# Optimization experiments

Measured on AMD Instinct MI355X. Metric: run time of the kernel, lower is better.

Reference implementation:

```python
import jax, jax.numpy as jnp
import numpy as np

N_TAXA = 32   # N taxa
K = 256       # particles
T = 16        # live subtrees at this step (t = N - r)
R = 16        # merges already done
S = 1024      # alignment sites
A = 4         # DNA alphabet
D = 64        # embedding dim
C = 16        # site-position feature dim
PRIOR_LEN = 0.1


def _expm4(M):
    """Matrix exponential of [..., A, A] via scaling-and-squaring + Taylor."""
    n_sq = 6
    Ms = M / (2.0 ** n_sq)
    I = jnp.eye(M.shape[-1], dtype=M.dtype)
    P = I + Ms
    Tm = Ms
    for i in range(2, 7):
        Tm = jnp.matmul(Tm, Ms) / i
        P = P + Tm
    for _ in range(n_sq):
        P = jnp.matmul(P, P)
    return P


def _stat_probs(emb_ExD, site_SxC, W_stat, W_site):
    # q_matrix_decoder.stat_probs_VxSxA: per-node, per-site stationary probs
    logits = emb_ExD @ W_stat                     # [E, A]
    logits = logits[:, None, :] + site_SxC @ W_site  # [E, S, A]
    return jax.nn.softmax(logits, axis=-1)


def setup_inputs() -> dict:
    key = jax.random.key(0)
    ks = jax.random.split(key, 10)
    ldf = np.zeros(2 * N_TAXA, np.float32)
    for n in range(2, 2 * N_TAXA):
        ldf[n] = ldf[n - 2] + np.log(n)
    return {
        "log_weight_K": jax.random.normal(ks[0], (K,), jnp.float32),
        "branch1_lengths_Kxr": jax.random.uniform(ks[1], (K, R), jnp.float32) * 0.2 + 1e-3,
        "branch2_lengths_Kxr": jax.random.uniform(ks[2], (K, R), jnp.float32) * 0.2 + 1e-3,
        "leaf_counts_Kxt": jnp.ones((K, T), jnp.int32),
        "embeddings_KxtxD": jax.random.normal(ks[3], (K, T, D), jnp.float32),
        "log_felsensteins_KxtxSxA": jax.nn.log_softmax(
            jax.random.normal(ks[4], (K, T, S, A), jnp.float32), axis=-1),
        "log_pi_K": jax.random.normal(ks[5], (K,), jnp.float32),
        "site_positions_SxC": jax.random.uniform(ks[6], (S, C), jnp.float32),
        "W_stat": jax.random.normal(ks[7], (D, A), jnp.float32) * 0.1,
        "W_site": jax.random.normal(ks[8], (C, A), jnp.float32) * 0.1,
        "log_double_factorials_2N": jnp.asarray(ldf),
    }


def reference(log_weight_K, branch1_lengths_Kxr, branch2_lengths_Kxr,
              leaf_counts_Kxt, embeddings_KxtxD, log_felsensteins_KxtxSxA,
              log_pi_K, site_positions_SxC, W_stat, W_site,
              log_double_factorials_2N):
    K_, T_, S_, A_ = log_felsensteins_KxtxSxA.shape
    key = jax.random.key(42)
    kres, ki, koff, ku1, ku2 = jax.random.split(key, 5)

    # ---- SMC categorical resampling over particles ----
    idxK = jax.random.categorical(kres, log_weight_K, shape=(K_,))
    b1r = branch1_lengths_Kxr[idxK]
    b2r = branch2_lengths_Kxr[idxK]
    lc = leaf_counts_Kxt[idxK]
    emb = embeddings_KxtxD[idxK]
    logf = log_felsensteins_KxtxSxA[idxK]
    prev_log_pi = log_pi_K[idxK]

    # ---- proposal (J=1): uniform pair + exponential branch lengths ----
    i = jax.random.randint(ki, (K_,), 0, T_)
    off = jax.random.randint(koff, (K_,), 1, T_)
    j = (i + off) % T_
    idx1 = jnp.minimum(i, j)
    idx2 = jnp.maximum(i, j)
    branch1 = -PRIOR_LEN * jnp.log(jax.random.uniform(ku1, (K_,), minval=1e-6, maxval=1.0))
    branch2 = -PRIOR_LEN * jnp.log(jax.random.uniform(ku2, (K_,), minval=1e-6, maxval=1.0))
    ar = jnp.arange(K_)
    new_emb = 0.5 * (emb[ar, idx1] + emb[ar, idx2])  # [K, D]
    log_v_plus = jnp.log(T_ * (T_ - 1) / 2.0)        # log #pairs

    # ---- merge: put merged value at idx1, move last slot into idx2, drop last ----
    def merge(arr, new_val):
        arr = arr.at[ar, idx1].set(new_val)
        arr = arr.at[ar, idx2].set(arr[ar, T_ - 1])
        return arr[:, :T_ - 1]

    lc_new = merge(lc, lc[ar, idx1] + lc[ar, idx2])   # [K, t-1]
    emb_new = merge(emb, new_emb)                     # [K, t-1, D]

    # ---- Felsenstein pruning step for the merged node ----
    stat = _stat_probs(new_emb, site_positions_SxC, W_stat, W_site)  # [K,S,A]
    Q = jnp.broadcast_to(stat[:, :, None, :], (K_, S_, A_, A_)) - jnp.eye(A_, dtype=stat.dtype)
    P1 = _expm4(Q * branch1[:, None, None, None])  # [K,S,A,A]
    P2 = _expm4(Q * branch2[:, None, None, None])
    f1 = jnp.exp(logf[ar, idx1])  # [K,S,A]
    f2 = jnp.exp(logf[ar, idx2])
    new_logf = (jnp.log(jnp.einsum('ksab,ksb->ksa', P1, f1) + 1e-30)
                + jnp.log(jnp.einsum('ksab,ksb->ksa', P2, f2) + 1e-30))
    logf_new = merge(logf, new_logf)  # [K, t-1, S, A]

    # ---- log pi over the forest: per-subtree likelihood + priors ----
    t_new = T_ - 1
    stat_all = _stat_probs(emb_new.reshape(K_ * t_new, -1), site_positions_SxC,
                           W_stat, W_site).reshape(K_, t_new, S_, A_)
    log_stat = jnp.log(stat_all)
    L = jnp.sum(jax.scipy.special.logsumexp(logf_new + log_stat, axis=-1), axis=-1)  # [K,t-1]
    topo_idx = jnp.clip(2 * lc_new - 3, 0, 2 * N_TAXA - 1)
    topo = -log_double_factorials_2N[topo_idx] * (lc_new >= 2).astype(L.dtype)
    b1_all = jnp.concatenate([b1r, branch1[:, None]], axis=1)  # [K, r+1]
    b2_all = jnp.concatenate([b2r, branch2[:, None]], axis=1)
    prior = (jnp.sum(-b1_all / PRIOR_LEN, axis=1) + jnp.sum(-b2_all / PRIOR_LEN, axis=1)
             - 2.0 * (b1_all.shape[1]) * jnp.log(jnp.asarray(PRIOR_LEN, L.dtype)))
    log_pi_new = jnp.sum(L + topo, axis=1) + prior

    # ---- importance weight ----
    log_v_minus = jnp.log(jnp.maximum(jnp.sum((lc_new > 1).astype(L.dtype), axis=1), 1.0))
    log_weight_new = log_pi_new - prev_log_pi + log_v_minus - log_v_plus
    return log_weight_new
```

## Files before the change

kernel.cpp:

```cpp
#include <hip/hip_runtime.h>
#include <stdint.h>


#define TF_ROT(x0,x1,r) { x0 += x1; x1 = ((x1<<(r))|(x1>>(32-(r)))); x1 ^= x0; }

__host__ __device__ inline void tf2x32(uint32_t k0, uint32_t k1,
                                       uint32_t x0, uint32_t x1,
                                       uint32_t& o0, uint32_t& o1) {
  uint32_t ks2 = k0 ^ k1 ^ 0x1BD11BDAu;
  x0 += k0; x1 += k1;
  TF_ROT(x0,x1,13) TF_ROT(x0,x1,15) TF_ROT(x0,x1,26) TF_ROT(x0,x1,6)
  x0 += k1; x1 += ks2 + 1u;
  TF_ROT(x0,x1,17) TF_ROT(x0,x1,29) TF_ROT(x0,x1,16) TF_ROT(x0,x1,24)
  x0 += ks2; x1 += k0 + 2u;
  TF_ROT(x0,x1,13) TF_ROT(x0,x1,15) TF_ROT(x0,x1,26) TF_ROT(x0,x1,6)
  x0 += k0; x1 += k1 + 3u;
  TF_ROT(x0,x1,17) TF_ROT(x0,x1,29) TF_ROT(x0,x1,16) TF_ROT(x0,x1,24)
  x0 += k1; x1 += ks2 + 4u;
  TF_ROT(x0,x1,13) TF_ROT(x0,x1,15) TF_ROT(x0,x1,26) TF_ROT(x0,x1,6)
  x0 += ks2; x1 += k0 + 5u;
  o0 = x0; o1 = x1;
}

struct Keys {
  uint32_t kres0, kres1;
  uint32_t k2i0, k2i1;
  uint32_t k1o0, k1o1;
  uint32_t k2o0, k2o1;
  uint32_t ku10, ku11;
  uint32_t ku20, ku21;
};

__device__ inline uint32_t rb_fold(uint32_t k0, uint32_t k1, uint32_t i) {
  uint32_t o0, o1;
  tf2x32(k0, k1, 0u, i, o0, o1);
  return o0 ^ o1;
}

__device__ inline float u01f(uint32_t b) {
  return __uint_as_float((b >> 9) | 0x3F800000u) - 1.0f;
}

#define TINYF 1.17549435e-38f

__global__ __launch_bounds__(256) void k_sf(
    const float* __restrict__ logw, const float* __restrict__ b1r,
    const float* __restrict__ b2r, const int* __restrict__ lc,
    const float* __restrict__ emb, const float* __restrict__ logpi,
    const float* __restrict__ Wstat, const float* __restrict__ ldf,
    const float* __restrict__ site, const float* __restrict__ Wsite,
    float* __restrict__ eslw, float* __restrict__ enlm,
    float* __restrict__ w1w, float* __restrict__ w2w,
    float* __restrict__ cw, int* __restrict__ pw, int* __restrict__ i1w,
    int* __restrict__ i2w, Keys kk) {
  int b = blockIdx.x, tid = threadIdx.x;
  if (b >= 256) {
    int s = (b - 256) * 256 + tid;
    float a0 = 0.f, a1 = 0.f, a2 = 0.f, a3 = 0.f;
#pragma unroll
    for (int c = 0; c < 16; c++) {
      float sc = site[s * 16 + c];
      a0 += sc * Wsite[c * 4 + 0];
      a1 += sc * Wsite[c * 4 + 1];
      a2 += sc * Wsite[c * 4 + 2];
      a3 += sc * Wsite[c * 4 + 3];
    }
    float4 v; v.x = __expf(a0); v.y = __expf(a1); v.z = __expf(a2); v.w = __expf(a3);
    ((float4*)eslw)[s] = v;
    return;
  }
  int k = b;
  __shared__ float sval[256];
  __shared__ int   sidx[256];
  __shared__ int   sh_i1, sh_i2;

  {
    uint32_t bb = rb_fold(kk.kres0, kk.kres1, (uint32_t)(k * 256 + tid));
    float u = fmaxf(TINYF, u01f(bb) + TINYF);
    float g = -logf(-logf(u));
    sval[tid] = g + logw[tid];
    sidx[tid] = tid;
  }
  __syncthreads();
  for (int st = 128; st > 0; st >>= 1) {
    if (tid < st) {
      float va = sval[tid], vb = sval[tid + st];
      int ia = sidx[tid], ib = sidx[tid + st];
      if (vb > va || (vb == va && ib < ia)) { sval[tid] = vb; sidx[tid] = ib; }
    }
    __syncthreads();
  }
  int p = sidx[0];

  if (tid == 0) {
    uint32_t i = rb_fold(kk.k2i0, kk.k2i1, (uint32_t)k) & 15u;
    uint32_t h = rb_fold(kk.k1o0, kk.k1o1, (uint32_t)k) % 15u;
    uint32_t l = rb_fold(kk.k2o0, kk.k2o1, (uint32_t)k) % 15u;
    uint32_t off = 1u + (h + l) % 15u;
    uint32_t j = (i + off) & 15u;
    int i1 = (int)(i < j ? i : j);
    int i2 = (int)(i < j ? j : i);
    sh_i1 = i1; sh_i2 = i2;

    const float SUBR = 1.0f - 1e-6f;
    float u1 = fmaxf(1e-6f, u01f(rb_fold(kk.ku10, kk.ku11, (uint32_t)k)) * SUBR + 1e-6f);
    float u2 = fmaxf(1e-6f, u01f(rb_fold(kk.ku20, kk.ku21, (uint32_t)k)) * SUBR + 1e-6f);
    float b1 = -0.1f * logf(u1);
    float b2 = -0.1f * logf(u2);
    w1w[k] = 1.0f - expf(-b1);
    w2w[k] = 1.0f - expf(-b2);
    i1w[k] = i1; i2w[k] = i2; pw[k] = p;

    float sb = b1 + b2;
    for (int r = 0; r < 16; r++) sb += b1r[p * 16 + r] + b2r[p * 16 + r];
    float prior = -sb / 0.1f - 34.0f * logf(0.1f);

    float topo_sum = 0.0f; int cnt = 0;
    for (int t = 0; t < 15; t++) {
      int lct;
      if (t == i1)      lct = lc[p * 16 + i1] + lc[p * 16 + i2];
      else if (t == i2) lct = lc[p * 16 + 15];
      else              lct = lc[p * 16 + t];
      int ti = 2 * lct - 3; ti = ti < 0 ? 0 : (ti > 63 ? 63 : ti);
      if (lct >= 2) topo_sum -= ldf[ti];
      if (lct > 1) cnt++;
    }
    float log_v_minus = logf(fmaxf((float)cnt, 1.0f));
    float log_v_plus = logf(120.0f);
    cw[k] = prior + topo_sum - logpi[p] + log_v_minus - log_v_plus;
  }
  __syncthreads();

  if (tid < 4) {
    int a = tid, i1 = sh_i1, i2 = sh_i2, p2 = sidx[0];
    const float* e1 = emb + ((size_t)p2 * 16 + i1) * 64;
    const float* e2 = emb + ((size_t)p2 * 16 + i2) * 64;
    float acc = 0.0f;
    for (int d = 0; d < 64; d++) acc += 0.5f * (e1[d] + e2[d]) * Wstat[d * 4 + a];
    enlm[k * 4 + a] = __expf(acc);
  }
}

__global__ __launch_bounds__(256) void k_lorig(
    const float* __restrict__ lfg, const float* __restrict__ eslw,
    const float* __restrict__ emb, const float* __restrict__ Wstat,
    const int* __restrict__ pw, const int* __restrict__ i1w,
    const int* __restrict__ i2w, const float* __restrict__ w1w,
    const float* __restrict__ w2w, const float* __restrict__ enlm,
    float* __restrict__ Lpart, float* __restrict__ Lm) {
  int p = blockIdx.y, sblk = blockIdx.x, tid = threadIdx.x;
  __shared__ int klist[256];
  __shared__ int kcount;
  __shared__ float enl[64];
  __shared__ float sred[16 * 4];
  __shared__ float sredm[4];
  if (tid == 0) kcount = 0;
  __syncthreads();
  if (pw[tid] == p) { int sl = atomicAdd(&kcount, 1); klist[sl] = tid; }
  __syncthreads();
  if (kcount == 0) return;

  if (tid < 64) {
    int t = tid >> 2, a = tid & 3;
    const float4* e4 = (const float4*)(emb + ((size_t)p * 16 + t) * 64);
    float acc = 0.0f;
#pragma unroll
    for (int d4 = 0; d4 < 16; d4++) {
      float4 e = e4[d4];
      acc += e.x * Wstat[(d4 * 4 + 0) * 4 + a] + e.y * Wstat[(d4 * 4 + 1) * 4 + a] +
             e.z * Wstat[(d4 * 4 + 2) * 4 + a] + e.w * Wstat[(d4 * 4 + 3) * 4 + a];
    }
    enl[tid] = __expf(acc);
  }
  __syncthreads();
  int s = sblk * 256 + tid;
  const float4 esl = ((const float4*)eslw)[s];
  const float* base = lfg + (size_t)p * 65536;

  float acc[16];
#pragma unroll
  for (int t = 0; t < 16; t++) {
    float4 lf = *(const float4*)(base + t * 4096 + s * 4);
    float w0 = enl[t * 4 + 0] * esl.x, w1 = enl[t * 4 + 1] * esl.y;
    float w2 = enl[t * 4 + 2] * esl.z, w3 = enl[t * 4 + 3] * esl.w;
    float S1 = w0 + w1 + w2 + w3;
    float S2 = __expf(lf.x) * w0 + __expf(lf.y) * w1 +
               __expf(lf.z) * w2 + __expf(lf.w) * w3;
    acc[t] = __log2f(S2) - __log2f(S1);
  }
#pragma unroll
  for (int t = 0; t < 16; t++) {
    float v = acc[t];
    for (int o = 32; o > 0; o >>= 1) v += __shfl_down(v, o, 64);
    if ((tid & 63) == 0) sred[t * 4 + (tid >> 6)] = v;
  }
  __syncthreads();
  if (tid < 16) {
    float s4 = sred[tid * 4 + 0] + sred[tid * 4 + 1] + sred[tid * 4 + 2] + sred[tid * 4 + 3];
    Lpart[((size_t)p * 4 + sblk) * 16 + tid] = s4 * 0.69314718056f;
  }

  for (int q = 0; q < kcount; q++) {
    int kq = klist[q];
    int i1 = i1w[kq], i2 = i2w[kq];
    float w1 = w1w[kq], w2 = w2w[kq];
    float om1 = 1.0f - w1, om2 = 1.0f - w2;
    float m0 = enlm[kq * 4 + 0], m1 = enlm[kq * 4 + 1];
    float m2 = enlm[kq * 4 + 2], m3 = enlm[kq * 4 + 3];
    float t0 = m0 * esl.x, t1 = m1 * esl.y, t2 = m2 * esl.z, t3 = m3 * esl.w;
    float T = t0 + t1 + t2 + t3;
    float invT = 1.0f / T;
    float4 lf1 = *(const float4*)(base + i1 * 4096 + s * 4);
    float4 lf2 = *(const float4*)(base + i2 * 4096 + s * 4);
    float f10 = __expf(lf1.x), f11 = __expf(lf1.y), f12 = __expf(lf1.z), f13 = __expf(lf1.w);
    float f20 = __expf(lf2.x), f21 = __expf(lf2.y), f22 = __expf(lf2.z), f23 = __expf(lf2.w);
    float dot1 = (t0 * f10 + t1 * f11 + t2 * f12 + t3 * f13) * invT;
    float dot2 = (t0 * f20 + t1 * f21 + t2 * f22 + t3 * f23) * invT;
    float n0 = __logf(om1 * f10 + w1 * dot1 + 1e-30f) + __logf(om2 * f20 + w2 * dot2 + 1e-30f);
    float n1 = __logf(om1 * f11 + w1 * dot1 + 1e-30f) + __logf(om2 * f21 + w2 * dot2 + 1e-30f);
    float n2 = __logf(om1 * f12 + w1 * dot1 + 1e-30f) + __logf(om2 * f22 + w2 * dot2 + 1e-30f);
    float n3 = __logf(om1 * f13 + w1 * dot1 + 1e-30f) + __logf(om2 * f23 + w2 * dot2 + 1e-30f);
    float S2 = __expf(n0) * t0 + __expf(n1) * t1 + __expf(n2) * t2 + __expf(n3) * t3;
    float tot = __logf(S2) - __logf(T);
    for (int o = 32; o > 0; o >>= 1) tot += __shfl_down(tot, o, 64);
    if ((tid & 63) == 0) sredm[tid >> 6] = tot;
    __syncthreads();
    if (tid == 0)
      Lm[kq * 4 + sblk] = sredm[0] + sredm[1] + sredm[2] + sredm[3];
    __syncthreads();
  }
}

__global__ __launch_bounds__(256) void k_out(
    const float* __restrict__ cw, const float* __restrict__ Lpart,
    const float* __restrict__ Lm, const int* __restrict__ pw,
    const int* __restrict__ i1w, const int* __restrict__ i2w,
    float* __restrict__ out) {
  int k = threadIdx.x;
  int p = pw[k], i1 = i1w[k], i2 = i2w[k];
  const float* Lp = Lpart + (size_t)p * 64;
  float sum = cw[k];
#pragma unroll
  for (int sb = 0; sb < 4; sb++) {
    float ss = Lm[k * 4 + sb];
    for (int t = 0; t < 16; t++)
      if (t != i1 && t != i2) ss += Lp[sb * 16 + t];
    sum += ss;
  }
  out[k] = sum;
}

extern "C" void kernel_launch(void* const* d_in, const int* in_sizes, int n_in,
                              void* d_out, int out_size, void* d_ws, size_t ws_size,
                              hipStream_t stream) {
  const float* logw  = (const float*)d_in[0];
  const float* b1r   = (const float*)d_in[1];
  const float* b2r   = (const float*)d_in[2];
  const int*   lc    = (const int*)d_in[3];
  const float* emb   = (const float*)d_in[4];
  const float* lfg   = (const float*)d_in[5];
  const float* logpi = (const float*)d_in[6];
  const float* site  = (const float*)d_in[7];
  const float* Wstat = (const float*)d_in[8];
  const float* Wsite = (const float*)d_in[9];
  const float* ldf   = (const float*)d_in[10];

  char* w = (char*)d_ws;
  float* eslw  = (float*)w; w += 1024 * 4 * 4;
  float* enlm  = (float*)w; w += 256 * 4 * 4;
  float* w1w   = (float*)w; w += 256 * 4;
  float* w2w   = (float*)w; w += 256 * 4;
  float* cw    = (float*)w; w += 256 * 4;
  int*   pw    = (int*)w;   w += 256 * 4;
  int*   i1w   = (int*)w;   w += 256 * 4;
  int*   i2w   = (int*)w;   w += 256 * 4;
  float* Lpart = (float*)w; w += 256 * 64 * 4;
  float* Lm    = (float*)w; w += 256 * 4 * 4;

  uint32_t S0[5], S1[5];
  for (uint32_t i = 0; i < 5; i++) tf2x32(0u, 42u, 0u, i, S0[i], S1[i]);
  Keys kk;
  kk.kres0 = S0[0]; kk.kres1 = S1[0];
  kk.ku10  = S0[3]; kk.ku11  = S1[3];
  kk.ku20  = S0[4]; kk.ku21  = S1[4];
  {
    uint32_t a0, a1, b0, b1;
    tf2x32(S0[1], S1[1], 0u, 0u, a0, a1);
    tf2x32(S0[1], S1[1], 0u, 1u, b0, b1);
    (void)a0; (void)a1;
    kk.k2i0 = b0; kk.k2i1 = b1;
  }
  {
    uint32_t a0, a1, b0, b1;
    tf2x32(S0[2], S1[2], 0u, 0u, a0, a1);
    tf2x32(S0[2], S1[2], 0u, 1u, b0, b1);
    kk.k1o0 = a0; kk.k1o1 = a1;
    kk.k2o0 = b0; kk.k2o1 = b1;
  }

  k_sf<<<260, 256, 0, stream>>>(logw, b1r, b2r, lc, emb, logpi, Wstat, ldf,
                                site, Wsite, eslw, enlm, w1w, w2w, cw,
                                pw, i1w, i2w, kk);
  dim3 gC(4, 256);
  k_lorig<<<gC, 256, 0, stream>>>(lfg, eslw, emb, Wstat, pw, i1w, i2w,
                                  w1w, w2w, enlm, Lpart, Lm);
  k_out<<<1, 256, 0, stream>>>(cw, Lpart, Lm, pw, i1w, i2w, (float*)d_out);
}
```

Baseline: 141.9 us.

## Move per-particle merged-subtree likelihood into dedicated blocks instead of serial loop

```diff
diff --git a/kernel.cpp b/kernel.cpp
--- a/kernel.cpp
+++ b/kernel.cpp
@@ -141,24 +141,60 @@
   }
 }
 
-__global__ __launch_bounds__(256) void k_lorig(
+__global__ __launch_bounds__(256) void k_mid(
     const float* __restrict__ lfg, const float* __restrict__ eslw,
     const float* __restrict__ emb, const float* __restrict__ Wstat,
     const int* __restrict__ pw, const int* __restrict__ i1w,
     const int* __restrict__ i2w, const float* __restrict__ w1w,
     const float* __restrict__ w2w, const float* __restrict__ enlm,
     float* __restrict__ Lpart, float* __restrict__ Lm) {
-  int p = blockIdx.y, sblk = blockIdx.x, tid = threadIdx.x;
-  __shared__ int klist[256];
-  __shared__ int kcount;
+  int tid = threadIdx.x;
+  if (blockIdx.x == 4) {
+    int k = blockIdx.y;
+    __shared__ float sredm[4];
+    int p = pw[k], i1 = i1w[k], i2 = i2w[k];
+    float w1 = w1w[k], w2 = w2w[k];
+    float om1 = 1.0f - w1, om2 = 1.0f - w2;
+    float m0 = enlm[k * 4 + 0], m1 = enlm[k * 4 + 1];
+    float m2 = enlm[k * 4 + 2], m3 = enlm[k * 4 + 3];
+    const float* base = lfg + (size_t)p * 65536;
+    float tot = 0.0f;
+#pragma unroll
+    for (int c = 0; c < 4; c++) {
+      int s = c * 256 + tid;
+      const float4 esl = ((const float4*)eslw)[s];
+      float t0 = m0 * esl.x, t1 = m1 * esl.y, t2 = m2 * esl.z, t3 = m3 * esl.w;
+      float T = t0 + t1 + t2 + t3;
+      float invT = 1.0f / T;
+      float4 lf1 = *(const float4*)(base + i1 * 4096 + s * 4);
+      float4 lf2 = *(const float4*)(base + i2 * 4096 + s * 4);
+      float f10 = __expf(lf1.x), f11 = __expf(lf1.y), f12 = __expf(lf1.z), f13 = __expf(lf1.w);
+      float f20 = __expf(lf2.x), f21 = __expf(lf2.y), f22 = __expf(lf2.z), f23 = __expf(lf2.w);
+      float dot1 = (t0 * f10 + t1 * f11 + t2 * f12 + t3 * f13) * invT;
+      float dot2 = (t0 * f20 + t1 * f21 + t2 * f22 + t3 * f23) * invT;
+      float n0 = __logf(om1 * f10 + w1 * dot1 + 1e-30f) + __logf(om2 * f20 + w2 * dot2 + 1e-30f);
+      float n1 = __logf(om1 * f11 + w1 * dot1 + 1e-30f) + __logf(om2 * f21 + w2 * dot2 + 1e-30f);
+      float n2 = __logf(om1 * f12 + w1 * dot1 + 1e-30f) + __logf(om2 * f22 + w2 * dot2 + 1e-30f);
+      float n3 = __logf(om1 * f13 + w1 * dot1 + 1e-30f) + __logf(om2 * f23 + w2 * dot2 + 1e-30f);
+      float S2 = __expf(n0) * t0 + __expf(n1) * t1 + __expf(n2) * t2 + __expf(n3) * t3;
+      tot += __logf(S2) - __logf(T);
+    }
+    for (int o = 32; o > 0; o >>= 1) tot += __shfl_down(tot, o, 64);
+    if ((tid & 63) == 0) sredm[tid >> 6] = tot;
+    __syncthreads();
+    if (tid == 0) Lm[k] = sredm[0] + sredm[1] + sredm[2] + sredm[3];
+    return;
+  }
+
+  int p = blockIdx.y, sblk = blockIdx.x;
+  __shared__ int kused;
   __shared__ float enl[64];
   __shared__ float sred[16 * 4];
-  __shared__ float sredm[4];
-  if (tid == 0) kcount = 0;
-  __syncthreads();
-  if (pw[tid] == p) { int sl = atomicAdd(&kcount, 1); klist[sl] = tid; }
-  __syncthreads();
-  if (kcount == 0) return;
+  if (tid == 0) kused = 0;
+  __syncthreads();
+  if (pw[tid] == p) kused = 1;
+  __syncthreads();
+  if (kused == 0) return;
 
   if (tid < 64) {
     int t = tid >> 2, a = tid & 3;
@@ -199,36 +235,6 @@
     float s4 = sred[tid * 4 + 0] + sred[tid * 4 + 1] + sred[tid * 4 + 2] + sred[tid * 4 + 3];
     Lpart[((size_t)p * 4 + sblk) * 16 + tid] = s4 * 0.69314718056f;
   }
-
-  for (int q = 0; q < kcount; q++) {
-    int kq = klist[q];
-    int i1 = i1w[kq], i2 = i2w[kq];
-    float w1 = w1w[kq], w2 = w2w[kq];
-    float om1 = 1.0f - w1, om2 = 1.0f - w2;
-    float m0 = enlm[kq * 4 + 0], m1 = enlm[kq * 4 + 1];
-    float m2 = enlm[kq * 4 + 2], m3 = enlm[kq * 4 + 3];
-    float t0 = m0 * esl.x, t1 = m1 * esl.y, t2 = m2 * esl.z, t3 = m3 * esl.w;
-    float T = t0 + t1 + t2 + t3;
-    float invT = 1.0f / T;
-    float4 lf1 = *(const float4*)(base + i1 * 4096 + s * 4);
-    float4 lf2 = *(const float4*)(base + i2 * 4096 + s * 4);
-    float f10 = __expf(lf1.x), f11 = __expf(lf1.y), f12 = __expf(lf1.z), f13 = __expf(lf1.w);
-    float f20 = __expf(lf2.x), f21 = __expf(lf2.y), f22 = __expf(lf2.z), f23 = __expf(lf2.w);
-    float dot1 = (t0 * f10 + t1 * f11 + t2 * f12 + t3 * f13) * invT;
-    float dot2 = (t0 * f20 + t1 * f21 + t2 * f22 + t3 * f23) * invT;
-    float n0 = __logf(om1 * f10 + w1 * dot1 + 1e-30f) + __logf(om2 * f20 + w2 * dot2 + 1e-30f);
-    float n1 = __logf(om1 * f11 + w1 * dot1 + 1e-30f) + __logf(om2 * f21 + w2 * dot2 + 1e-30f);
-    float n2 = __logf(om1 * f12 + w1 * dot1 + 1e-30f) + __logf(om2 * f22 + w2 * dot2 + 1e-30f);
-    float n3 = __logf(om1 * f13 + w1 * dot1 + 1e-30f) + __logf(om2 * f23 + w2 * dot2 + 1e-30f);
-    float S2 = __expf(n0) * t0 + __expf(n1) * t1 + __expf(n2) * t2 + __expf(n3) * t3;
-    float tot = __logf(S2) - __logf(T);
-    for (int o = 32; o > 0; o >>= 1) tot += __shfl_down(tot, o, 64);
-    if ((tid & 63) == 0) sredm[tid >> 6] = tot;
-    __syncthreads();
-    if (tid == 0)
-      Lm[kq * 4 + sblk] = sredm[0] + sredm[1] + sredm[2] + sredm[3];
-    __syncthreads();
-  }
 }
 
 __global__ __launch_bounds__(256) void k_out(
@@ -239,10 +245,10 @@
   int k = threadIdx.x;
   int p = pw[k], i1 = i1w[k], i2 = i2w[k];
   const float* Lp = Lpart + (size_t)p * 64;
-  float sum = cw[k];
+  float sum = cw[k] + Lm[k];
 #pragma unroll
   for (int sb = 0; sb < 4; sb++) {
-    float ss = Lm[k * 4 + sb];
+    float ss = 0.0f;
     for (int t = 0; t < 16; t++)
       if (t != i1 && t != i2) ss += Lp[sb * 16 + t];
     sum += ss;
@@ -275,7 +281,7 @@
   int*   i1w   = (int*)w;   w += 256 * 4;
   int*   i2w   = (int*)w;   w += 256 * 4;
   float* Lpart = (float*)w; w += 256 * 64 * 4;
-  float* Lm    = (float*)w; w += 256 * 4 * 4;
+  float* Lm    = (float*)w; w += 256 * 4;
 
   uint32_t S0[5], S1[5];
   for (uint32_t i = 0; i < 5; i++) tf2x32(0u, 42u, 0u, i, S0[i], S1[i]);
@@ -301,8 +307,8 @@
   k_sf<<<260, 256, 0, stream>>>(logw, b1r, b2r, lc, emb, logpi, Wstat, ldf,
                                 site, Wsite, eslw, enlm, w1w, w2w, cw,
                                 pw, i1w, i2w, kk);
-  dim3 gC(4, 256);
-  k_lorig<<<gC, 256, 0, stream>>>(lfg, eslw, emb, Wstat, pw, i1w, i2w,
-                                  w1w, w2w, enlm, Lpart, Lm);
+  dim3 gM(5, 256);
+  k_mid<<<gM, 256, 0, stream>>>(lfg, eslw, emb, Wstat, pw, i1w, i2w,
+                                w1w, w2w, enlm, Lpart, Lm);
   k_out<<<1, 256, 0, stream>>>(cw, Lpart, Lm, pw, i1w, i2w, (float*)d_out);
 }
```

Measured after the change: 134.1 us. 1.06x faster.
